# Kernel tuning notes

Measured on AMD Instinct MI355X. Metric: run time of the kernel, lower is better.

Reference implementation:

```python
import jax, jax.numpy as jnp
import numpy as np

DN = ('NCHW', 'OIHW', 'NCHW')


def conv2d(x, w, b, pad=1):
    y = jax.lax.conv_general_dilated(x, w, window_strides=(1, 1),
                                     padding=[(pad, pad), (pad, pad)],
                                     dimension_numbers=DN)
    return y + b[None, :, None, None]


def deform_conv2d(x, offset, w, b):
    """Deformable conv v1 (torchvision layout): offset [B, 2*K*K, H, W],
    channel 2k = dy_k, 2k+1 = dx_k, kernel points row-major."""
    B, C, H, W = x.shape
    K = 3
    off = offset.reshape(B, K * K, 2, H, W)
    dy, dx = off[:, :, 0], off[:, :, 1]            # [B,9,H,W]
    ky = jnp.repeat(jnp.arange(K) - 1, K).astype(x.dtype)   # row-major kernel grid
    kx = jnp.tile(jnp.arange(K) - 1, K).astype(x.dtype)
    hh = jnp.arange(H, dtype=x.dtype)
    ww = jnp.arange(W, dtype=x.dtype)
    py = hh[None, None, :, None] + ky[None, :, None, None] + dy  # [B,9,H,W]
    px = ww[None, None, None, :] + kx[None, :, None, None] + dx

    y0 = jnp.floor(py)
    x0 = jnp.floor(px)
    ly, lx = py - y0, px - x0
    y0i, x0i = y0.astype(jnp.int32), x0.astype(jnp.int32)

    def gather(yi, xi):
        valid = ((yi >= 0) & (yi < H) & (xi >= 0) & (xi < W))
        yc = jnp.clip(yi, 0, H - 1)
        xc = jnp.clip(xi, 0, W - 1)
        # per-batch fancy gather: [C,H,W] indexed by [9,H,W] -> [C,9,H,W]
        g = jax.vmap(lambda xb, yy, xx: xb[:, yy, xx])(x, yc, xc)  # [B,C,9,H,W]
        return g * valid[:, None].astype(x.dtype)

    w00 = ((1 - ly) * (1 - lx))[:, None]
    w01 = ((1 - ly) * lx)[:, None]
    w10 = (ly * (1 - lx))[:, None]
    w11 = (ly * lx)[:, None]
    val = (gather(y0i, x0i) * w00 + gather(y0i, x0i + 1) * w01 +
           gather(y0i + 1, x0i) * w10 + gather(y0i + 1, x0i + 1) * w11)  # [B,C,9,H,W]

    wk = w.reshape(w.shape[0], C * K * K)                 # [Cout, C*9]
    out = jnp.einsum('bkhw,ok->bohw', val.reshape(B, C * K * K, H, W), wk)
    return out + b[None, :, None, None]


def setup_inputs() -> dict:
    key = jax.random.key(0)
    k1, k2, k3, k4 = jax.random.split(key, 4)
    B, Cin, Cout, H, W = 8, 128, 256, 64, 64
    fan = 1.0 / np.sqrt(Cin * 9)
    return {
        'x': jax.random.normal(k1, (B, Cin, H, W), jnp.float32),
        'w_off': jax.random.normal(k2, (18, Cin, 3, 3), jnp.float32) * 0.01,
        'b_off': jnp.zeros((18,), jnp.float32),
        'w_def': jax.random.normal(k3, (Cout, Cin, 3, 3), jnp.float32) * fan,
        'b_def': jax.random.normal(k4, (Cout,), jnp.float32) * 0.01,
    }


def reference(x, w_off, b_off, w_def, b_def):
    offset = conv2d(x, w_off, b_off, pad=1)
    y = deform_conv2d(x, offset, w_def, b_def)
    return jax.nn.relu(y)
```

## Files before the change

kernel.cpp:

```cpp
#include <hip/hip_runtime.h>
#include <hip/hip_bf16.h>

#define HH 64
#define WW 64
#define CIN 128
#define COUT 256
#define KK 1152
#define TP 32
#define PW 66
#define XTIMG (PW*PW*CIN)
#define RS 264

typedef short bf16x8 __attribute__((ext_vector_type(8)));
typedef float f32x4  __attribute__((ext_vector_type(4)));

__device__ inline short f2bf(float f) {
    union { float f; unsigned u; } v; v.f = f;
    unsigned r = v.u + 0x7FFFu + ((v.u >> 16) & 1u);
    return (short)(r >> 16);
}
__device__ inline float bf2f(ushort u) {
    union { unsigned u; float f; } v; v.u = (unsigned)u << 16; return v.f;
}

__global__ __launch_bounds__(256) void transpose_x(const float* __restrict__ x,
                                                   ushort* __restrict__ xt) {
    int hp = blockIdx.x;
    int b  = blockIdx.y;
    int t  = threadIdx.x;
    ushort* row = xt + ((size_t)b * PW + hp) * PW * CIN;
    if (hp == 0 || hp == PW - 1) {
        ushort4 z4 = {0, 0, 0, 0};
        for (int f = t; f < 2112; f += 256) ((ushort4*)row)[f] = z4;
        return;
    }
    __shared__ short tl[66 * 132];
    int h = hp - 1;
    if (t < 128) { tl[t] = 0; tl[65 * 132 + t] = 0; }
    const float* xbh = x + (((size_t)b * CIN) << 12) + (h << 6);
#pragma unroll
    for (int it = 0; it < 8; it++) {
        int c  = it * 16 + (t >> 4);
        int w4 = (t & 15) * 4;
        float4 v = *(const float4*)(xbh + ((size_t)c << 12) + w4);
        tl[(w4 + 1) * 132 + c] = f2bf(v.x);
        tl[(w4 + 2) * 132 + c] = f2bf(v.y);
        tl[(w4 + 3) * 132 + c] = f2bf(v.z);
        tl[(w4 + 4) * 132 + c] = f2bf(v.w);
    }
    __syncthreads();
    for (int f = t; f < 2112; f += 256) {
        int wp = f >> 5, c4 = (f & 31) * 4;
        const short* s = &tl[wp * 132 + c4];
        ushort4 v; v.x = s[0]; v.y = s[1]; v.z = s[2]; v.w = s[3];
        ((ushort4*)row)[f] = v;
    }
}

__global__ void cast_wall(const float* __restrict__ wd, const float* __restrict__ wo,
                          short* __restrict__ wf, short* __restrict__ wfo) {
    int ks = blockIdx.x, m = blockIdx.y, l = threadIdx.x;
    bf16x8 v;
    if (m < 16) {
        int co = m * 16 + (l & 15);
#pragma unroll
        for (int j = 0; j < 8; j++) {
            int ckp = ks * 32 + ((l >> 4) << 3) + j;
            int c = ckp & 127, k = ckp >> 7;
            v[j] = f2bf(wd[(size_t)co * KK + c * 9 + k]);
        }
        *(bf16x8*)(wf + ((size_t)(m * 36 + ks) * 64 + l) * 8) = v;
    } else {
        int mm = m - 16;
        int co = mm * 16 + (l & 15);
#pragma unroll
        for (int j = 0; j < 8; j++) {
            int ckp = ks * 32 + ((l >> 4) << 3) + j;
            int c = ckp & 127, k = ckp >> 7;
            v[j] = (co < 18) ? f2bf(wo[(size_t)co * KK + c * 9 + k]) : (short)0;
        }
        *(bf16x8*)(wfo + ((size_t)(mm * 36 + ks) * 64 + l) * 8) = v;
    }
}

__global__ __launch_bounds__(256, 3) void fused_deform(const ushort* __restrict__ xt,
                                                       const short* __restrict__ wf,
                                                       const short* __restrict__ wfo,
                                                       const float* __restrict__ bo,
                                                       const float* __restrict__ bias,
                                                       float* __restrict__ out) {
    __shared__ short   s_raw[64 * RS];
    __shared__ short   s_val[TP][128];
    __shared__ float   s_off[18][TP];
    __shared__ float4  s_w[9][TP];
    __shared__ ushort2 s_o[9][TP];

    int t = threadIdx.x, bi = blockIdx.x;
    int b = bi & 7, h = (bi >> 3) & 63, tile = bi >> 9, w0 = tile * TP;
    const ushort* xb = xt + (size_t)b * XTIMG;
    int wv = t >> 6, l = t & 63, lane16 = l & 15, quad = l >> 4;

    {
        short* sv0 = s_raw;
        short* sv1 = s_raw + 4096;
        int cpix = t >> 3;
        int g0 = 2 * (t & 7), g1 = g0 + 1;
        int gs0 = (g0 ^ (cpix & 15)) * 8, gs1 = (g1 ^ (cpix & 15)) * 8;
        bf16x8 r0, r1;
        auto oload = [&](int k) {
            const ushort* base = xb + ((size_t)(h + k / 3) * PW + w0 + k % 3) * CIN;
            r0 = *(const bf16x8*)(base + t * 16);
            r1 = *(const bf16x8*)(base + t * 16 + 8);
        };
        auto ostore = [&](int buf) {
            short* sv = buf ? sv1 : sv0;
            *(bf16x8*)(sv + cpix * 128 + gs0) = r0;
            *(bf16x8*)(sv + cpix * 128 + gs1) = r1;
        };
        int mt = wv >> 1, nt = wv & 1;
        f32x4 aoff = {0.f, 0.f, 0.f, 0.f};
        const short* Ab = wfo + (size_t)l * 8 + (size_t)mt * 36 * 512;

        oload(0); ostore(0);
        __syncthreads();
        for (int k = 0; k < 9; k++) {
            if (k < 8) oload(k + 1);
            const short* sv = (k & 1) ? sv1 : sv0;
#pragma unroll
            for (int ksp = 0; ksp < 4; ksp++) {
                bf16x8 a  = *(const bf16x8*)(Ab + (k * 4 + ksp) * 512);
                bf16x8 bf = *(const bf16x8*)(sv + (nt * 16 + lane16) * 128 + ((ksp * 4 + quad) ^ lane16) * 8);
                aoff = __builtin_amdgcn_mfma_f32_16x16x32_bf16(a, bf, aoff, 0, 0, 0);
            }
            if (k < 8) ostore((k + 1) & 1);
            __syncthreads();
        }
        int cob = mt * 16 + quad * 4;
#pragma unroll
        for (int r = 0; r < 4; r++) {
            int co = cob + r;
            if (co < 18) s_off[co][nt * 16 + lane16] = aoff[r] + bo[co];
        }
    }
    __syncthreads();

    for (int jj = t; jj < 9 * TP; jj += 256) {
        int k = jj >> 5, pixj = jj & 31, wp = w0 + pixj;
        float dy = s_off[2 * k][pixj];
        float dx = s_off[2 * k + 1][pixj];
        float py = (float)(h + k / 3 - 1) + dy;
        float px = (float)(wp + k % 3 - 1) + dx;
        float y0f = floorf(py), x0f = floorf(px);
        float ly = py - y0f, lx = px - x0f;
        int y0 = (int)y0f, x0 = (int)x0f;
        float a0, a1;
        if (x0 >= 0 && x0 <= 62)      { a0 = 1.f - lx; a1 = lx; }
        else if (x0 == -1)            { a0 = lx;       a1 = 0.f; }
        else if (x0 == 63)            { a0 = 0.f;      a1 = 1.f - lx; }
        else                          { a0 = 0.f;      a1 = 0.f; }
        int xb0 = min(max(x0, 0), 62);
        bool vy0 = (y0 >= 0) && (y0 < HH);
        bool vy1 = (y0 >= -1) && (y0 < HH - 1);
        int y0c = min(max(y0, 0), HH - 1);
        int y1c = min(max(y0 + 1, 0), HH - 1);
        float wy0 = (1.f - ly) * (vy0 ? 1.f : 0.f);
        float wy1 = ly * (vy1 ? 1.f : 0.f);
        s_o[k][pixj] = make_ushort2((ushort)((y0c + 1) * PW + xb0 + 1),
                                    (ushort)((y1c + 1) * PW + xb0 + 1));
        s_w[k][pixj] = make_float4(wy0 * a0, wy0 * a1, wy1 * a0, wy1 * a1);
    }
    __syncthreads();

    int g = t >> 2, sub = t & 3;
    int gpix = g & 31, gr = g >> 5;
    bf16x8 rv[8];
    auto gload = [&](int k) {
        ushort2 o = s_o[k][gpix];
        int loc = gr ? o.y : o.x;
        const ushort* p = xb + (size_t)loc * CIN + sub * 8;
#pragma unroll
        for (int i = 0; i < 8; i++) rv[i] = *(const bf16x8*)(p + i * 32);
    };
    auto gstore = [&]() {
        short* d = s_raw + g * RS + sub * 8;
#pragma unroll
        for (int i = 0; i < 8; i++) *(bf16x8*)(d + i * 32) = rv[i];
    };
    int cpix2 = t & 31, cg = t >> 5;
    auto combine = [&](int k) {
        float4 w4 = s_w[k][cpix2];
        const short* r0b = s_raw + cpix2 * RS;
        const short* r1b = s_raw + (cpix2 + 32) * RS;
#pragma unroll
        for (int j2 = 0; j2 < 2; j2++) {
            int ch = cg * 16 + j2 * 8;
            bf16x8 c00 = *(const bf16x8*)(r0b + ch);
            bf16x8 c01 = *(const bf16x8*)(r0b + 128 + ch);
            bf16x8 c10 = *(const bf16x8*)(r1b + ch);
            bf16x8 c11 = *(const bf16x8*)(r1b + 128 + ch);
            bf16x8 fr;
#pragma unroll
            for (int i = 0; i < 8; i++) {
                float v = w4.x * bf2f((ushort)c00[i]) + w4.y * bf2f((ushort)c01[i])
                        + w4.z * bf2f((ushort)c10[i]) + w4.w * bf2f((ushort)c11[i]);
                fr[i] = f2bf(v);
            }
            *(bf16x8*)&s_val[cpix2][((cg * 2 + j2) ^ (cpix2 & 15)) * 8] = fr;
        }
    };

    f32x4 z = {0.f, 0.f, 0.f, 0.f};
    f32x4 acc[4][2];
#pragma unroll
    for (int i = 0; i < 4; i++)
#pragma unroll
        for (int j = 0; j < 2; j++) acc[i][j] = z;
    const short* Aw = wf + (size_t)l * 8;

    gload(0);
    gstore();
    __syncthreads();
    combine(0);
    gload(1);
    __syncthreads();

    for (int k = 0; k < 9; k++) {
#pragma unroll
        for (int ksp = 0; ksp < 4; ksp++) {
            int ks = k * 4 + ksp;
            int gsw = ((ksp * 4 + quad) ^ lane16) * 8;
            bf16x8 b0 = *(const bf16x8*)&s_val[lane16     ][gsw];
            bf16x8 b1 = *(const bf16x8*)&s_val[16 + lane16][gsw];
            bf16x8 a0 = *(const bf16x8*)(Aw + (size_t)((wv * 4 + 0) * 36 + ks) * 512);
            bf16x8 a1 = *(const bf16x8*)(Aw + (size_t)((wv * 4 + 1) * 36 + ks) * 512);
            bf16x8 a2 = *(const bf16x8*)(Aw + (size_t)((wv * 4 + 2) * 36 + ks) * 512);
            bf16x8 a3 = *(const bf16x8*)(Aw + (size_t)((wv * 4 + 3) * 36 + ks) * 512);
            acc[0][0] = __builtin_amdgcn_mfma_f32_16x16x32_bf16(a0, b0, acc[0][0], 0, 0, 0);
            acc[1][0] = __builtin_amdgcn_mfma_f32_16x16x32_bf16(a1, b0, acc[1][0], 0, 0, 0);
            acc[2][0] = __builtin_amdgcn_mfma_f32_16x16x32_bf16(a2, b0, acc[2][0], 0, 0, 0);
            acc[3][0] = __builtin_amdgcn_mfma_f32_16x16x32_bf16(a3, b0, acc[3][0], 0, 0, 0);
            acc[0][1] = __builtin_amdgcn_mfma_f32_16x16x32_bf16(a0, b1, acc[0][1], 0, 0, 0);
            acc[1][1] = __builtin_amdgcn_mfma_f32_16x16x32_bf16(a1, b1, acc[1][1], 0, 0, 0);
            acc[2][1] = __builtin_amdgcn_mfma_f32_16x16x32_bf16(a2, b1, acc[2][1], 0, 0, 0);
            acc[3][1] = __builtin_amdgcn_mfma_f32_16x16x32_bf16(a3, b1, acc[3][1], 0, 0, 0);
        }
        if (k < 8) {
            gstore();
            __syncthreads();
            combine(k + 1);
            if (k < 7) gload(k + 2);
            __syncthreads();
        }
    }

#pragma unroll
    for (int ct = 0; ct < 4; ct++) {
        int co = wv * 64 + ct * 16 + quad * 4;
#pragma unroll
        for (int pt = 0; pt < 2; pt++) {
            int colx = w0 + pt * 16 + lane16;
#pragma unroll
            for (int rr = 0; rr < 4; rr++) {
                float v = acc[ct][pt][rr] + bias[co + rr];
                out[(((size_t)b * COUT + co + rr) << 12) + (h << 6) + colx] = fmaxf(v, 0.f);
            }
        }
    }
}

extern "C" void kernel_launch(void* const* d_in, const int* in_sizes, int n_in,
                              void* d_out, int out_size, void* d_ws, size_t ws_size,
                              hipStream_t stream) {
    const float* x     = (const float*)d_in[0];
    const float* w_off = (const float*)d_in[1];
    const float* b_off = (const float*)d_in[2];
    const float* w_def = (const float*)d_in[3];
    const float* b_def = (const float*)d_in[4];
    float* out = (float*)d_out;

    short*  wf  = (short*)d_ws;
    short*  wfo = wf + (size_t)16 * 36 * 512;
    ushort* xt  = (ushort*)(wfo + (size_t)2 * 36 * 512);

    transpose_x<<<dim3(PW, 8), 256, 0, stream>>>(x, xt);
    cast_wall<<<dim3(36, 18), 64, 0, stream>>>(w_def, w_off, wf, wfo);
    fused_deform<<<1024, 256, 0, stream>>>(xt, wf, wfo, b_off, b_def, out);
}
```

Before: 135.3 us.

## Merge prep kernels, widen tile to full row, gather-combine in registers

Merges the input transpose and the weight cast into one prep launch. The fused kernel now processes a full 64-pixel row per block instead of 32, so each weight fragment is reused across four pixel tiles. The offset conv reads its B operands straight from global memory instead of staging them in LDS. The bilinear gather loads the four corners into registers and blends them there with packed bf16 conversion, dropping the raw LDS staging buffer and a barrier per kernel tap. In exchange there are fewer blocks (512), occupancy drops to 2 blocks per CU, and register pressure rises.

```diff
diff --git a/kernel.cpp b/kernel.cpp
--- a/kernel.cpp
+++ b/kernel.cpp
@@ -6,10 +6,8 @@
 #define CIN 128
 #define COUT 256
 #define KK 1152
-#define TP 32
 #define PW 66
 #define XTIMG (PW*PW*CIN)
-#define RS 264
 
 typedef short bf16x8 __attribute__((ext_vector_type(8)));
 typedef float f32x4  __attribute__((ext_vector_type(4)));
@@ -19,15 +17,54 @@
     unsigned r = v.u + 0x7FFFu + ((v.u >> 16) & 1u);
     return (short)(r >> 16);
 }
-__device__ inline float bf2f(ushort u) {
-    union { unsigned u; float f; } v; v.u = (unsigned)u << 16; return v.f;
-}
-
-__global__ __launch_bounds__(256) void transpose_x(const float* __restrict__ x,
-                                                   ushort* __restrict__ xt) {
-    int hp = blockIdx.x;
-    int b  = blockIdx.y;
-    int t  = threadIdx.x;
+__device__ inline float lo16(unsigned u) {
+    union { unsigned u; float f; } v; v.u = u << 16; return v.f;
+}
+__device__ inline float hi16(unsigned u) {
+    union { unsigned u; float f; } v; v.u = u & 0xffff0000u; return v.f;
+}
+__device__ inline unsigned pk2(float lo, float hi) {
+    union { __hip_bfloat162 h; unsigned u; } c;
+    c.h = __float22bfloat162_rn(make_float2(lo, hi));
+    return c.u;
+}
+
+__global__ __launch_bounds__(256) void prep(const float* __restrict__ x,
+                                            const float* __restrict__ wd,
+                                            const float* __restrict__ wo,
+                                            ushort* __restrict__ xt,
+                                            short* __restrict__ wf,
+                                            short* __restrict__ wfo) {
+    int bi = blockIdx.x, t = threadIdx.x;
+    if (bi >= 528) {
+        int flat = (bi - 528) * 256 + t;
+        int m = flat / 2304;
+        int r = flat - m * 2304;
+        int ks = r >> 6, l = r & 63;
+        bf16x8 v;
+        if (m < 16) {
+            int co = m * 16 + (l & 15);
+#pragma unroll
+            for (int j = 0; j < 8; j++) {
+                int ckp = ks * 32 + ((l >> 4) << 3) + j;
+                int c = ckp & 127, k = ckp >> 7;
+                v[j] = f2bf(wd[(size_t)co * KK + c * 9 + k]);
+            }
+            *(bf16x8*)(wf + ((size_t)(m * 36 + ks) * 64 + l) * 8) = v;
+        } else {
+            int mm = m - 16;
+            int co = mm * 16 + (l & 15);
+#pragma unroll
+            for (int j = 0; j < 8; j++) {
+                int ckp = ks * 32 + ((l >> 4) << 3) + j;
+                int c = ckp & 127, k = ckp >> 7;
+                v[j] = (co < 18) ? f2bf(wo[(size_t)co * KK + c * 9 + k]) : (short)0;
+            }
+            *(bf16x8*)(wfo + ((size_t)(mm * 36 + ks) * 64 + l) * 8) = v;
+        }
+        return;
+    }
+    int hp = bi % 66, b = bi / 66;
     ushort* row = xt + ((size_t)b * PW + hp) * PW * CIN;
     if (hp == 0 || hp == PW - 1) {
         ushort4 z4 = {0, 0, 0, 0};
@@ -57,95 +94,52 @@
     }
 }
 
-__global__ void cast_wall(const float* __restrict__ wd, const float* __restrict__ wo,
-                          short* __restrict__ wf, short* __restrict__ wfo) {
-    int ks = blockIdx.x, m = blockIdx.y, l = threadIdx.x;
-    bf16x8 v;
-    if (m < 16) {
-        int co = m * 16 + (l & 15);
-#pragma unroll
-        for (int j = 0; j < 8; j++) {
-            int ckp = ks * 32 + ((l >> 4) << 3) + j;
-            int c = ckp & 127, k = ckp >> 7;
-            v[j] = f2bf(wd[(size_t)co * KK + c * 9 + k]);
-        }
-        *(bf16x8*)(wf + ((size_t)(m * 36 + ks) * 64 + l) * 8) = v;
-    } else {
-        int mm = m - 16;
-        int co = mm * 16 + (l & 15);
-#pragma unroll
-        for (int j = 0; j < 8; j++) {
-            int ckp = ks * 32 + ((l >> 4) << 3) + j;
-            int c = ckp & 127, k = ckp >> 7;
-            v[j] = (co < 18) ? f2bf(wo[(size_t)co * KK + c * 9 + k]) : (short)0;
-        }
-        *(bf16x8*)(wfo + ((size_t)(mm * 36 + ks) * 64 + l) * 8) = v;
-    }
-}
-
-__global__ __launch_bounds__(256, 3) void fused_deform(const ushort* __restrict__ xt,
+__global__ __launch_bounds__(256, 2) void fused_deform(const ushort* __restrict__ xt,
                                                        const short* __restrict__ wf,
                                                        const short* __restrict__ wfo,
                                                        const float* __restrict__ bo,
                                                        const float* __restrict__ bias,
                                                        float* __restrict__ out) {
-    __shared__ short   s_raw[64 * RS];
-    __shared__ short   s_val[TP][128];
-    __shared__ float   s_off[18][TP];
-    __shared__ float4  s_w[9][TP];
-    __shared__ ushort2 s_o[9][TP];
+    __shared__ short   s_val[64][128];
+    __shared__ float4  s_w[9][64];
+    __shared__ ushort2 s_o[9][64];
+    __shared__ float   s_off[18][64];
 
     int t = threadIdx.x, bi = blockIdx.x;
-    int b = bi & 7, h = (bi >> 3) & 63, tile = bi >> 9, w0 = tile * TP;
+    int b = bi & 7, h = bi >> 3;
     const ushort* xb = xt + (size_t)b * XTIMG;
     int wv = t >> 6, l = t & 63, lane16 = l & 15, quad = l >> 4;
 
     {
-        short* sv0 = s_raw;
-        short* sv1 = s_raw + 4096;
-        int cpix = t >> 3;
-        int g0 = 2 * (t & 7), g1 = g0 + 1;
-        int gs0 = (g0 ^ (cpix & 15)) * 8, gs1 = (g1 ^ (cpix & 15)) * 8;
-        bf16x8 r0, r1;
-        auto oload = [&](int k) {
-            const ushort* base = xb + ((size_t)(h + k / 3) * PW + w0 + k % 3) * CIN;
-            r0 = *(const bf16x8*)(base + t * 16);
-            r1 = *(const bf16x8*)(base + t * 16 + 8);
-        };
-        auto ostore = [&](int buf) {
-            short* sv = buf ? sv1 : sv0;
-            *(bf16x8*)(sv + cpix * 128 + gs0) = r0;
-            *(bf16x8*)(sv + cpix * 128 + gs1) = r1;
-        };
-        int mt = wv >> 1, nt = wv & 1;
-        f32x4 aoff = {0.f, 0.f, 0.f, 0.f};
-        const short* Ab = wfo + (size_t)l * 8 + (size_t)mt * 36 * 512;
-
-        oload(0); ostore(0);
-        __syncthreads();
+        f32x4 aoff0 = {0.f, 0.f, 0.f, 0.f}, aoff1 = aoff0;
+        const short* A0 = wfo + (size_t)l * 8;
+        const short* A1 = wfo + (size_t)36 * 512 + l * 8;
+        int pix0 = lane16 + 16 * wv;
+#pragma unroll 1
         for (int k = 0; k < 9; k++) {
-            if (k < 8) oload(k + 1);
-            const short* sv = (k & 1) ? sv1 : sv0;
+            const ushort* bbase = xb + ((size_t)(h + k / 3) * PW + pix0 + k % 3) * CIN + quad * 8;
 #pragma unroll
             for (int ksp = 0; ksp < 4; ksp++) {
-                bf16x8 a  = *(const bf16x8*)(Ab + (k * 4 + ksp) * 512);
-                bf16x8 bf = *(const bf16x8*)(sv + (nt * 16 + lane16) * 128 + ((ksp * 4 + quad) ^ lane16) * 8);
-                aoff = __builtin_amdgcn_mfma_f32_16x16x32_bf16(a, bf, aoff, 0, 0, 0);
-            }
-            if (k < 8) ostore((k + 1) & 1);
-            __syncthreads();
-        }
-        int cob = mt * 16 + quad * 4;
+                int ks = k * 4 + ksp;
+                bf16x8 bfr = *(const bf16x8*)(bbase + ksp * 32);
+                bf16x8 af0 = *(const bf16x8*)(A0 + (size_t)ks * 512);
+                bf16x8 af1 = *(const bf16x8*)(A1 + (size_t)ks * 512);
+                aoff0 = __builtin_amdgcn_mfma_f32_16x16x32_bf16(af0, bfr, aoff0, 0, 0, 0);
+                aoff1 = __builtin_amdgcn_mfma_f32_16x16x32_bf16(af1, bfr, aoff1, 0, 0, 0);
+            }
+        }
 #pragma unroll
         for (int r = 0; r < 4; r++) {
-            int co = cob + r;
-            if (co < 18) s_off[co][nt * 16 + lane16] = aoff[r] + bo[co];
+            int co = quad * 4 + r;
+            s_off[co][pix0] = aoff0[r] + bo[co];
+            int co1 = co + 16;
+            if (co1 < 18) s_off[co1][pix0] = aoff1[r] + bo[co1];
         }
     }
     __syncthreads();
 
-    for (int jj = t; jj < 9 * TP; jj += 256) {
-        int k = jj >> 5, pixj = jj & 31, wp = w0 + pixj;
+    for (int jj = t; jj < 576; jj += 256) {
+        int k = jj >> 6, pixj = jj & 63, wp = pixj;
         float dy = s_off[2 * k][pixj];
         float dx = s_off[2 * k + 1][pixj];
         float py = (float)(h + k / 3 - 1) + dy;
@@ -169,99 +163,90 @@
                                     (ushort)((y1c + 1) * PW + xb0 + 1));
         s_w[k][pixj] = make_float4(wy0 * a0, wy0 * a1, wy1 * a0, wy1 * a1);
     }
+
+    int gpix = t >> 2, sub = t & 3;
+    const ushort* xg = xb + sub * 8;
+    bf16x8 cur[4];
+
+    auto gli = [&](int k) {
+        ushort2 o = s_o[k][gpix];
+        float4 w4 = s_w[k][gpix];
+        const ushort* p0 = xg + (size_t)o.x * CIN;
+        const ushort* p1 = xg + (size_t)o.y * CIN;
+        uint4 c00[4], c01[4], c10[4], c11[4];
+#pragma unroll
+        for (int i = 0; i < 4; i++) {
+            c00[i] = *(const uint4*)(p0 + i * 32);
+            c01[i] = *(const uint4*)(p0 + 128 + i * 32);
+            c10[i] = *(const uint4*)(p1 + i * 32);
+            c11[i] = *(const uint4*)(p1 + 128 + i * 32);
+        }
+#pragma unroll
+        for (int i = 0; i < 4; i++) {
+            uint4 o4;
+            const unsigned* u00 = (const unsigned*)&c00[i];
+            const unsigned* u01 = (const unsigned*)&c01[i];
+            const unsigned* u10 = (const unsigned*)&c10[i];
+            const unsigned* u11 = (const unsigned*)&c11[i];
+            unsigned* ov = (unsigned*)&o4;
+#pragma unroll
+            for (int d = 0; d < 4; d++) {
+                float vl = w4.x * lo16(u00[d]) + w4.y * lo16(u01[d])
+                         + w4.z * lo16(u10[d]) + w4.w * lo16(u11[d]);
+                float vh = w4.x * hi16(u00[d]) + w4.y * hi16(u01[d])
+                         + w4.z * hi16(u10[d]) + w4.w * hi16(u11[d]);
+                ov[d] = pk2(vl, vh);
+            }
+            cur[i] = *(bf16x8*)&o4;
+        }
+    };
+
+    f32x4 z = {0.f, 0.f, 0.f, 0.f};
+    f32x4 acc[4][4];
+#pragma unroll
+    for (int i = 0; i < 4; i++)
+#pragma unroll
+        for (int j = 0; j < 4; j++) acc[i][j] = z;
+    const short* Aw = wf + (size_t)l * 8;
+
     __syncthreads();
-
-    int g = t >> 2, sub = t & 3;
-    int gpix = g & 31, gr = g >> 5;
-    bf16x8 rv[8];
-    auto gload = [&](int k) {
-        ushort2 o = s_o[k][gpix];
-        int loc = gr ? o.y : o.x;
-        const ushort* p = xb + (size_t)loc * CIN + sub * 8;
-#pragma unroll
-        for (int i = 0; i < 8; i++) rv[i] = *(const bf16x8*)(p + i * 32);
-    };
-    auto gstore = [&]() {
-        short* d = s_raw + g * RS + sub * 8;
-#pragma unroll
-        for (int i = 0; i < 8; i++) *(bf16x8*)(d + i * 32) = rv[i];
-    };
-    int cpix2 = t & 31, cg = t >> 5;
-    auto combine = [&](int k) {
-        float4 w4 = s_w[k][cpix2];
-        const short* r0b = s_raw + cpix2 * RS;
-        const short* r1b = s_raw + (cpix2 + 32) * RS;
-#pragma unroll
-        for (int j2 = 0; j2 < 2; j2++) {
-            int ch = cg * 16 + j2 * 8;
-            bf16x8 c00 = *(const bf16x8*)(r0b + ch);
-            bf16x8 c01 = *(const bf16x8*)(r0b + 128 + ch);
-            bf16x8 c10 = *(const bf16x8*)(r1b + ch);
-            bf16x8 c11 = *(const bf16x8*)(r1b + 128 + ch);
-            bf16x8 fr;
-#pragma unroll
-            for (int i = 0; i < 8; i++) {
-                float v = w4.x * bf2f((ushort)c00[i]) + w4.y * bf2f((ushort)c01[i])
-                        + w4.z * bf2f((ushort)c10[i]) + w4.w * bf2f((ushort)c11[i]);
-                fr[i] = f2bf(v);
-            }
-            *(bf16x8*)&s_val[cpix2][((cg * 2 + j2) ^ (cpix2 & 15)) * 8] = fr;
-        }
-    };
-
-    f32x4 z = {0.f, 0.f, 0.f, 0.f};
-    f32x4 acc[4][2];
-#pragma unroll
-    for (int i = 0; i < 4; i++)
-#pragma unroll
-        for (int j = 0; j < 2; j++) acc[i][j] = z;
-    const short* Aw = wf + (size_t)l * 8;
-
-    gload(0);
-    gstore();
-    __syncthreads();
-    combine(0);
-    gload(1);
-    __syncthreads();
+    gli(0);
 
     for (int k = 0; k < 9; k++) {
+#pragma unroll
+        for (int i = 0; i < 4; i++)
+            *(bf16x8*)&s_val[gpix][((((i << 2) + sub) ^ (gpix & 15)) << 3)] = cur[i];
+        __syncthreads();
+        if (k < 8) gli(k + 1);
 #pragma unroll
         for (int ksp = 0; ksp < 4; ksp++) {
             int ks = k * 4 + ksp;
-            int gsw = ((ksp * 4 + quad) ^ lane16) * 8;
-            bf16x8 b0 = *(const bf16x8*)&s_val[lane16     ][gsw];
-            bf16x8 b1 = *(const bf16x8*)&s_val[16 + lane16][gsw];
-            bf16x8 a0 = *(const bf16x8*)(Aw + (size_t)((wv * 4 + 0) * 36 + ks) * 512);
-            bf16x8 a1 = *(const bf16x8*)(Aw + (size_t)((wv * 4 + 1) * 36 + ks) * 512);
-            bf16x8 a2 = *(const bf16x8*)(Aw + (size_t)((wv * 4 + 2) * 36 + ks) * 512);
-            bf16x8 a3 = *(const bf16x8*)(Aw + (size_t)((wv * 4 + 3) * 36 + ks) * 512);
-            acc[0][0] = __builtin_amdgcn_mfma_f32_16x16x32_bf16(a0, b0, acc[0][0], 0, 0, 0);
-            acc[1][0] = __builtin_amdgcn_mfma_f32_16x16x32_bf16(a1, b0, acc[1][0], 0, 0, 0);
-            acc[2][0] = __builtin_amdgcn_mfma_f32_16x16x32_bf16(a2, b0, acc[2][0], 0, 0, 0);
-            acc[3][0] = __builtin_amdgcn_mfma_f32_16x16x32_bf16(a3, b0, acc[3][0], 0, 0, 0);
-            acc[0][1] = __builtin_amdgcn_mfma_f32_16x16x32_bf16(a0, b1, acc[0][1], 0, 0, 0);
-            acc[1][1] = __builtin_amdgcn_mfma_f32_16x16x32_bf16(a1, b1, acc[1][1], 0, 0, 0);
-            acc[2][1] = __builtin_amdgcn_mfma_f32_16x16x32_bf16(a2, b1, acc[2][1], 0, 0, 0);
-            acc[3][1] = __builtin_amdgcn_mfma_f32_16x16x32_bf16(a3, b1, acc[3][1], 0, 0, 0);
-        }
-        if (k < 8) {
-            gstore();
-            __syncthreads();
-            combine(k + 1);
-            if (k < 7) gload(k + 2);
-            __syncthreads();
-        }
-    }
-
-#pragma unroll
-    for (int ct = 0; ct < 4; ct++) {
-        int co = wv * 64 + ct * 16 + quad * 4;
-#pragma unroll
-        for (int pt = 0; pt < 2; pt++) {
-            int colx = w0 + pt * 16 + lane16;
+            int gg = (ksp << 2) + quad;
+            bf16x8 b0 = *(const bf16x8*)&s_val[lane16     ][(gg ^ lane16) << 3];
+            bf16x8 b1 = *(const bf16x8*)&s_val[16 + lane16][(gg ^ lane16) << 3];
+            bf16x8 b2 = *(const bf16x8*)&s_val[32 + lane16][(gg ^ lane16) << 3];
+            bf16x8 b3 = *(const bf16x8*)&s_val[48 + lane16][(gg ^ lane16) << 3];
+#pragma unroll
+            for (int mt = 0; mt < 4; mt++) {
+                bf16x8 a = *(const bf16x8*)(Aw + (size_t)(((wv * 4 + mt) * 36) + ks) * 512);
+                acc[mt][0] = __builtin_amdgcn_mfma_f32_16x16x32_bf16(a, b0, acc[mt][0], 0, 0, 0);
+                acc[mt][1] = __builtin_amdgcn_mfma_f32_16x16x32_bf16(a, b1, acc[mt][1], 0, 0, 0);
+                acc[mt][2] = __builtin_amdgcn_mfma_f32_16x16x32_bf16(a, b2, acc[mt][2], 0, 0, 0);
+                acc[mt][3] = __builtin_amdgcn_mfma_f32_16x16x32_bf16(a, b3, acc[mt][3], 0, 0, 0);
+            }
+        }
+        __syncthreads();
+    }
+
+#pragma unroll
+    for (int mt = 0; mt < 4; mt++) {
+        int co = (wv * 4 + mt) * 16 + quad * 4;
+#pragma unroll
+        for (int nt = 0; nt < 4; nt++) {
+            int colx = nt * 16 + lane16;
 #pragma unroll
             for (int rr = 0; rr < 4; rr++) {
-                float v = acc[ct][pt][rr] + bias[co + rr];
+                float v = acc[mt][nt][rr] + bias[co + rr];
                 out[(((size_t)b * COUT + co + rr) << 12) + (h << 6) + colx] = fmaxf(v, 0.f);
             }
         }
@@ -282,7 +267,6 @@
     short*  wfo = wf + (size_t)16 * 36 * 512;
     ushort* xt  = (ushort*)(wfo + (size_t)2 * 36 * 512);
 
-    transpose_x<<<dim3(PW, 8), 256, 0, stream>>>(x, xt);
-    cast_wall<<<dim3(36, 18), 64, 0, stream>>>(w_def, w_off, wf, wfo);
-    fused_deform<<<1024, 256, 0, stream>>>(xt, wf, wfo, b_off, b_def, out);
-}
+    prep<<<690, 256, 0, stream>>>(x, w_def, w_off, xt, wf, wfo);
+    fused_deform<<<512, 256, 0, stream>>>(xt, wf, wfo, b_off, b_def, out);
+}
```

Result: slower. 140.5 us (+3.8%).
